# Kernel optimization log

Measured on AMD Instinct MI355X. Metric: run time of the kernel, lower is better.

The kernel has to match this reference:

```python
import jax, jax.numpy as jnp
import numpy as np

DIM = 64
K = 8
B_TAIL = 3.0
HIDDEN = 64
BATCH = 16384
MIN_BIN_WIDTH = 1e-3
MIN_BIN_HEIGHT = 1e-3
MIN_DERIVATIVE = 1e-3


def setup_inputs() -> dict:
    key = jax.random.key(0)
    ks = jax.random.split(key, 8)
    L = DIM - 1
    out_dim = 3 * K - 1
    def u(k, shape, fan_in):
        b = 1.0 / np.sqrt(fan_in)
        return jax.random.uniform(k, shape, minval=-b, maxval=b, dtype=jnp.float32)
    return {
        "x": jax.random.normal(ks[0], (BATCH, DIM), jnp.float32),
        "init_param": jax.random.uniform(ks[1], (out_dim,), minval=-0.5, maxval=0.5, dtype=jnp.float32),
        # conditioner MLP i (i=1..dim-1) maps x[:, :i] -> 3K-1; stacked with zero-masked inputs
        "W1": u(ks[2], (L, HIDDEN, DIM), DIM),
        "b1": u(ks[3], (L, HIDDEN), DIM),
        "W2": u(ks[4], (L, HIDDEN, HIDDEN), HIDDEN),
        "b2": u(ks[5], (L, HIDDEN), HIDDEN),
        "W3": u(ks[6], (L, out_dim, HIDDEN), HIDDEN),
        "b3": u(ks[7], (L, out_dim), HIDDEN),
    }


def _rqs(inputs, uW, uH, uD, left, right):
    # inputs: [D, B]; uW/uH: [D, B, K]; uD: [D, B, K+1] (already edge-padded)
    num_bins = uW.shape[-1]
    widths = jax.nn.softmax(uW, axis=-1)
    widths = MIN_BIN_WIDTH + (1 - MIN_BIN_WIDTH * num_bins) * widths
    cw = jnp.pad(jnp.cumsum(widths, axis=-1), ((0, 0), (0, 0), (1, 0)))
    cw = (right - left) * cw + left
    cw = cw.at[..., 0].set(left).at[..., -1].set(right)
    widths = cw[..., 1:] - cw[..., :-1]

    derivs = MIN_DERIVATIVE + jax.nn.softplus(uD)

    heights = jax.nn.softmax(uH, axis=-1)
    heights = MIN_BIN_HEIGHT + (1 - MIN_BIN_HEIGHT * num_bins) * heights
    ch = jnp.pad(jnp.cumsum(heights, axis=-1), ((0, 0), (0, 0), (1, 0)))
    ch = (right - left) * ch + left  # bottom=left, top=right (symmetric box)
    ch = ch.at[..., 0].set(left).at[..., -1].set(right)
    heights = ch[..., 1:] - ch[..., :-1]

    # searchsorted: sum(inputs >= bin_edges) - 1, with eps on last edge
    cw_s = cw.at[..., -1].add(1e-6)
    bin_idx = jnp.sum(inputs[..., None] >= cw_s, axis=-1) - 1
    bin_idx = jnp.clip(bin_idx, 0, num_bins - 1)[..., None]
    take = lambda a: jnp.take_along_axis(a, bin_idx, axis=-1)[..., 0]

    in_cw = take(cw)
    in_w = take(widths)
    in_ch = take(ch)
    in_h = take(heights)
    in_delta = take(heights / widths)
    d_k = take(derivs)
    d_k1 = take(derivs[..., 1:])

    theta = (inputs - in_cw) / in_w
    t1mt = theta * (1 - theta)
    numer = in_h * (in_delta * theta**2 + d_k * t1mt)
    denom = in_delta + (d_k + d_k1 - 2 * in_delta) * t1mt
    outputs = in_ch + numer / denom
    dnum = in_delta**2 * (d_k1 * theta**2 + 2 * in_delta * t1mt + d_k * (1 - theta) ** 2)
    logabsdet = jnp.log(dnum) - 2 * jnp.log(denom)
    return outputs, logabsdet


def _unconstrained_rqs(inputs, uW, uH, uD, tail_bound):
    inside = (inputs >= -tail_bound) & (inputs <= tail_bound)
    const = float(np.log(np.exp(1 - MIN_DERIVATIVE) - 1))
    uD = jnp.pad(uD, ((0, 0), (0, 0), (1, 1)), constant_values=const)
    x_in = jnp.clip(inputs, -tail_bound, tail_bound)
    out, ld = _rqs(x_in, uW, uH, uD, -tail_bound, tail_bound)
    return jnp.where(inside, out, inputs), jnp.where(inside, ld, 0.0)


def reference(x, init_param, W1, b1, W2, b2, W3, b3):
    Bsz = x.shape[0]
    L = DIM - 1
    # row l of mask keeps x[:, :l+1], zeroes the rest -> identical to per-layer x[:, :i]
    mask = jnp.tril(jnp.ones((L, DIM), x.dtype))
    xm = x[None, :, :] * mask[:, None, :]                         # [L, B, D]
    h = jnp.tanh(jnp.einsum('lbd,lhd->lbh', xm, W1) + b1[:, None, :])
    h = jnp.tanh(jnp.einsum('lbh,lgh->lbg', h, W2) + b2[:, None, :])
    out = jnp.einsum('lbh,loh->lbo', h, W3) + b3[:, None, :]      # [L, B, 3K-1]
    params = jnp.concatenate(
        [jnp.broadcast_to(init_param, (1, Bsz, 3 * K - 1)), out], axis=0)  # [D, B, 3K-1]
    W = 2 * B_TAIL * jax.nn.softmax(params[..., :K], axis=-1)
    H = 2 * B_TAIL * jax.nn.softmax(params[..., K:2 * K], axis=-1)
    Dp = jax.nn.softplus(params[..., 2 * K:])
    z_t, ld = _unconstrained_rqs(x.T, W, H, Dp, B_TAIL)           # [D, B]
    return z_t.T, ld.sum(axis=0)
```

## Files before the change

kernel.cpp:

```cpp
#include <hip/hip_runtime.h>

#define BATCH 16384
#define LAYERS 63
#define BM 128
#define XS 72
#define BLOB_BYTES 21504
#define LDS_OFF 8192
#define LDS_BYTES 13312

typedef float f4 __attribute__((ext_vector_type(4)));
typedef short s8 __attribute__((ext_vector_type(8)));
typedef unsigned int u4 __attribute__((ext_vector_type(4)));

#define LOG2E  1.442695041f
#define LN2    0.6931471806f

__device__ __forceinline__ float rcpf(float v) { return __builtin_amdgcn_rcpf(v); }

__device__ __forceinline__ float exp2_hw(float x) {
#if __has_builtin(__builtin_amdgcn_exp2f)
    return __builtin_amdgcn_exp2f(x);
#else
    return exp2f(x);
#endif
}

__device__ __forceinline__ float fast_tanh(float v) {
    float e = exp2_hw(v * (2.f * LOG2E));
    return 1.f - 2.f * rcpf(e + 1.f);
}
__device__ __forceinline__ float softplus_f(float v) {
    float e = exp2_hw(-fabsf(v) * LOG2E);
    return fmaxf(v, 0.f) + LN2 * __log2f(1.f + e);
}
__device__ __forceinline__ unsigned short f2bf(float f) {
    unsigned int u = __float_as_uint(f);
    u += 0x7fffu + ((u >> 16) & 1u);
    return (unsigned short)(u >> 16);
}
#if __has_builtin(__builtin_amdgcn_cvt_pk_bf16_f32)
__device__ __forceinline__ unsigned pk2(float a, float b) {
    auto r = __builtin_amdgcn_cvt_pk_bf16_f32(a, b);
    return __builtin_bit_cast(unsigned, r);
}
#else
__device__ __forceinline__ unsigned pk2(float a, float b) {
    return (unsigned)f2bf(a) | ((unsigned)f2bf(b) << 16);
}
#endif
__device__ __forceinline__ unsigned long long pack4(float a, float b, float c, float d) {
    return (unsigned long long)pk2(a, b) | ((unsigned long long)pk2(c, d) << 32);
}

__device__ __forceinline__ void rqs_eval(const float* p, float xv, float& zout, float& ldout) {
    const bool inside = (xv >= -3.f) && (xv <= 3.f);
    const float xi = fminf(fmaxf(xv, -3.f), 3.f);

    float wa[8], ha[8];
    {
        float s = 0.f;
        #pragma unroll
        for (int i = 0; i < 8; i++) { wa[i] = exp2_hw(p[i] * LOG2E); s += wa[i]; }
        float inv = 6.f * rcpf(s);
        #pragma unroll
        for (int i = 0; i < 8; i++) wa[i] *= inv;
        s = 0.f;
        #pragma unroll
        for (int i = 0; i < 8; i++) { wa[i] = exp2_hw(wa[i] * LOG2E); s += wa[i]; }
        inv = 0.992f * rcpf(s);
        #pragma unroll
        for (int i = 0; i < 8; i++) wa[i] = 1e-3f + wa[i] * inv;
    }
    {
        float s = 0.f;
        #pragma unroll
        for (int i = 0; i < 8; i++) { ha[i] = exp2_hw(p[8 + i] * LOG2E); s += ha[i]; }
        float inv = 6.f * rcpf(s);
        #pragma unroll
        for (int i = 0; i < 8; i++) ha[i] *= inv;
        s = 0.f;
        #pragma unroll
        for (int i = 0; i < 8; i++) { ha[i] = exp2_hw(ha[i] * LOG2E); s += ha[i]; }
        inv = 0.992f * rcpf(s);
        #pragma unroll
        for (int i = 0; i < 8; i++) ha[i] = 1e-3f + ha[i] * inv;
    }

    float cw[9], ch[9];
    cw[0] = -3.f; ch[0] = -3.f;
    {
        float cs = 0.f, hs = 0.f;
        #pragma unroll
        for (int k = 1; k < 8; k++) {
            cs += wa[k - 1]; cw[k] = 6.f * cs - 3.f;
            hs += ha[k - 1]; ch[k] = 6.f * hs - 3.f;
        }
    }
    cw[8] = 3.f; ch[8] = 3.f;

    int cnt = 0;
    #pragma unroll
    for (int k = 0; k < 8; k++) cnt += (xi >= cw[k]) ? 1 : 0;
    cnt += (xi >= 3.000001f) ? 1 : 0;
    const int bin = min(max(cnt - 1, 0), 7);

    float in_cw = 0.f, in_w = 1.f, in_ch = 0.f, in_h = 1.f;
    float pd0 = 0.f, pd1 = 0.f;
    #pragma unroll
    for (int k = 0; k < 8; k++)
        if (k == bin) {
            in_cw = cw[k]; in_w = cw[k + 1] - cw[k];
            in_ch = ch[k]; in_h = ch[k + 1] - ch[k];
            if (k >= 1) pd0 = p[15 + k];
            if (k <= 6) pd1 = p[16 + k];
        }
    const float dk  = (bin == 0) ? 1.f : 1e-3f + softplus_f(softplus_f(pd0));
    const float dk1 = (bin == 7) ? 1.f : 1e-3f + softplus_f(softplus_f(pd1));

    const float rw    = rcpf(in_w);
    const float delta = in_h * rw;
    const float th    = (xi - in_cw) * rw;
    const float omt = 1.f - th;
    const float t1  = th * omt;
    const float th2 = th * th;
    const float numer = in_h * (delta * th2 + dk * t1);
    const float denom = delta + (dk + dk1 - 2.f * delta) * t1;
    const float rd    = rcpf(denom);
    const float outv  = in_ch + numer * rd;
    const float dnum  = delta * delta * (dk1 * th2 + 2.f * delta * t1 + dk * omt * omt);
    const float ldv = LN2 * __log2f(dnum * rd * rd);

    zout  = inside ? outv : xv;
    ldout = inside ? ldv : 0.f;
}

__global__ __launch_bounds__(256) void prep_kernel(
    const float* __restrict__ x, const float* __restrict__ init_param,
    const float* __restrict__ W1, const float* __restrict__ W2, const float* __restrict__ W3,
    const float* __restrict__ b1, const float* __restrict__ b2, const float* __restrict__ b3,
    unsigned short* __restrict__ x_bf, unsigned char* __restrict__ blobG,
    float* __restrict__ z, float* __restrict__ ld)
{
    const int tid = threadIdx.x;
    if (blockIdx.x < 1024) {
        size_t idx = (size_t)blockIdx.x * 256 + tid;
        f4 v = *(const f4*)&x[idx * 4];
        *(unsigned long long*)&x_bf[idx * 4] = pack4(v[0], v[1], v[2], v[3]);
        return;
    }
    if (blockIdx.x >= 1024 + LAYERS) {
        const int row = (blockIdx.x - 1024 - LAYERS) * 256 + tid;
        float p[23];
        #pragma unroll
        for (int j = 0; j < 23; j++) p[j] = init_param[j];
        float zv, lv;
        rqs_eval(p, x[(size_t)row * 64], zv, lv);
        z[(size_t)row * 64] = zv;
        ld[row] = lv;
        return;
    }
    const int l = blockIdx.x - 1024;
    unsigned char* gb = blobG + (size_t)l * BLOB_BYTES;
    for (int e = tid; e < 1024; e += 256) {
        int m = e >> 9, r = (e >> 3) & 63, j = e & 7;
        const float* src = (m ? W2 : W1) + (size_t)l * 4096 + r * 64 + j * 8;
        unsigned long long lo = pack4(src[0], src[1], src[2], src[3]);
        unsigned long long hi = pack4(src[4], src[5], src[6], src[7]);
        unsigned long long* dst = (unsigned long long*)(gb + m * 8192 + r * 128 + ((j ^ (r & 7)) << 4));
        dst[0] = lo; dst[1] = hi;
    }
    if (tid < 256) {
        int r = tid >> 3, j = tid & 7;
        unsigned long long lo = 0ull, hi = 0ull;
        if (r < 23) {
            const float* src = W3 + (size_t)l * 1472 + r * 64 + j * 8;
            lo = pack4(src[0], src[1], src[2], src[3]);
            hi = pack4(src[4], src[5], src[6], src[7]);
        }
        unsigned long long* dst = (unsigned long long*)(gb + 16384 + r * 128 + ((j ^ (r & 7)) << 4));
        dst[0] = lo; dst[1] = hi;
    }
    if (tid < 64)        *(float*)(gb + 20480 + tid * 4)         = b1[l * 64 + tid];
    else if (tid < 128)  *(float*)(gb + 20736 + (tid - 64) * 4)  = b2[l * 64 + tid - 64];
    else if (tid < 160)  *(float*)(gb + 20992 + (tid - 128) * 4) = (tid - 128 < 23) ? b3[l * 23 + tid - 128] : 0.f;
    else                 { int e = tid - 160; if (e < 96) *(float*)(gb + 21120 + e * 4) = 0.f; }
}

__global__ __launch_bounds__(256, 5) void mlp_rqs_kernel(
    const float* __restrict__ x, const unsigned short* __restrict__ x_bf,
    const unsigned char* __restrict__ blobG,
    float* __restrict__ z, float* __restrict__ ld)
{
    const int l = blockIdx.y, keff = l + 1;
    const int b0 = blockIdx.x * BM;
    const int tid = threadIdx.x;
    const int ln = tid & 63, wv = tid >> 6;
    const int c = ln & 15, q = ln >> 4;
    const int mbase = wv * 32;
    const int c7 = c & 7;

    __shared__ __align__(16) unsigned char blob[LDS_BYTES];
    __shared__ __align__(16) unsigned short Hs[BM * XS];

    unsigned short* W2s = (unsigned short*)blob;
    unsigned short* W3s = (unsigned short*)(blob + 8192);
    const float* b1s = (const float*)(blob + 12288);
    const float* b2s = (const float*)(blob + 12544);
    const float* b3s = (const float*)(blob + 12800);
    float* PsF = (float*)Hs;

    const unsigned char* gblob = blobG + (size_t)l * BLOB_BYTES;

    for (int t = wv; t < 13; t += 4)
        __builtin_amdgcn_global_load_lds(
            (const __attribute__((address_space(1))) void*)(gblob + LDS_OFF + t * 1024 + ln * 16),
            (__attribute__((address_space(3))) void*)(blob + t * 1024 + ln * 16), 16, 0, 0);

    const int ks1 = (keff + 31) >> 5;

    s8 aw1[2][4];
    #pragma unroll
    for (int mt = 0; mt < 4; mt++)
        aw1[0][mt] = *(const s8*)(gblob + (mt * 16 + c) * 128 + ((q ^ c7) << 4));
    if (ks1 == 2) {
        #pragma unroll
        for (int mt = 0; mt < 4; mt++)
            aw1[1][mt] = *(const s8*)(gblob + (mt * 16 + c) * 128 + (((4 + q) ^ c7) << 4));
    }

    u4 B0u, B1u, B2u{}, B3u{};
    {
        const unsigned short* xr = x_bf + (size_t)(b0 + mbase + c) * 64 + q * 8;
        B0u = *(const u4*)xr;  B1u = *(const u4*)(xr + 1024);
        if (ks1 == 2) { B2u = *(const u4*)(xr + 32); B3u = *(const u4*)(xr + 1024 + 32); }
        const int n = keff - ((ks1 - 1) * 32 + q * 8);
        unsigned mk[4];
        #pragma unroll
        for (int i = 0; i < 4; i++) {
            int m = n - 2 * i;
            mk[i] = (m >= 2) ? 0xFFFFFFFFu : ((m == 1) ? 0xFFFFu : 0u);
        }
        if (ks1 == 2) {
            #pragma unroll
            for (int i = 0; i < 4; i++) { B2u[i] &= mk[i]; B3u[i] &= mk[i]; }
        } else {
            #pragma unroll
            for (int i = 0; i < 4; i++) { B0u[i] &= mk[i]; B1u[i] &= mk[i]; }
        }
    }
    const float xv = x[(size_t)(b0 + (tid & 127)) * 64 + keff];

    __syncthreads();

    {
        f4 acc[4][2];
        #pragma unroll
        for (int mt = 0; mt < 4; mt++) {
            f4 bv = *(const f4*)&b1s[mt * 16 + q * 4];
            acc[mt][0] = bv; acc[mt][1] = bv;
        }
        {
            s8 bx0 = __builtin_bit_cast(s8, B0u), bx1 = __builtin_bit_cast(s8, B1u);
            #pragma unroll
            for (int mt = 0; mt < 4; mt++) {
                acc[mt][0] = __builtin_amdgcn_mfma_f32_16x16x32_bf16(aw1[0][mt], bx0, acc[mt][0], 0, 0, 0);
                acc[mt][1] = __builtin_amdgcn_mfma_f32_16x16x32_bf16(aw1[0][mt], bx1, acc[mt][1], 0, 0, 0);
            }
        }
        if (ks1 == 2) {
            s8 bx0 = __builtin_bit_cast(s8, B2u), bx1 = __builtin_bit_cast(s8, B3u);
            #pragma unroll
            for (int mt = 0; mt < 4; mt++) {
                acc[mt][0] = __builtin_amdgcn_mfma_f32_16x16x32_bf16(aw1[1][mt], bx0, acc[mt][0], 0, 0, 0);
                acc[mt][1] = __builtin_amdgcn_mfma_f32_16x16x32_bf16(aw1[1][mt], bx1, acc[mt][1], 0, 0, 0);
            }
        }
        #pragma unroll
        for (int mt = 0; mt < 4; mt++)
            #pragma unroll
            for (int nt = 0; nt < 2; nt++) {
                f4 a = acc[mt][nt];
                unsigned long long w = (unsigned long long)pk2(fast_tanh(a[0]), fast_tanh(a[1]))
                    | ((unsigned long long)pk2(fast_tanh(a[2]), fast_tanh(a[3])) << 32);
                *(unsigned long long*)&Hs[(mbase + nt * 16 + c) * XS + mt * 16 + q * 4] = w;
            }
    }

    {
        f4 acc[4][2];
        #pragma unroll
        for (int mt = 0; mt < 4; mt++) {
            f4 bv = *(const f4*)&b2s[mt * 16 + q * 4];
            acc[mt][0] = bv; acc[mt][1] = bv;
        }
        #pragma unroll
        for (int ks = 0; ks < 2; ks++) {
            s8 bh0 = *(const s8*)&Hs[(mbase + c) * XS + ks * 32 + q * 8];
            s8 bh1 = *(const s8*)&Hs[(mbase + 16 + c) * XS + ks * 32 + q * 8];
            const int sb = ((ks * 4 + q) ^ c7) * 8;
            #pragma unroll
            for (int mt = 0; mt < 4; mt++) {
                s8 aw = *(const s8*)&W2s[(mt * 16 + c) * 64 + sb];
                acc[mt][0] = __builtin_amdgcn_mfma_f32_16x16x32_bf16(aw, bh0, acc[mt][0], 0, 0, 0);
                acc[mt][1] = __builtin_amdgcn_mfma_f32_16x16x32_bf16(aw, bh1, acc[mt][1], 0, 0, 0);
            }
        }
        #pragma unroll
        for (int mt = 0; mt < 4; mt++)
            #pragma unroll
            for (int nt = 0; nt < 2; nt++) {
                f4 a = acc[mt][nt];
                unsigned long long w = (unsigned long long)pk2(fast_tanh(a[0]), fast_tanh(a[1]))
                    | ((unsigned long long)pk2(fast_tanh(a[2]), fast_tanh(a[3])) << 32);
                *(unsigned long long*)&Hs[(mbase + nt * 16 + c) * XS + mt * 16 + q * 4] = w;
            }
    }

    {
        f4 acc3[2][2];
        #pragma unroll
        for (int mt = 0; mt < 2; mt++) {
            f4 bv = *(const f4*)&b3s[mt * 16 + q * 4];
            acc3[mt][0] = bv; acc3[mt][1] = bv;
        }
        #pragma unroll
        for (int ks = 0; ks < 2; ks++) {
            s8 bh0 = *(const s8*)&Hs[(mbase + c) * XS + ks * 32 + q * 8];
            s8 bh1 = *(const s8*)&Hs[(mbase + 16 + c) * XS + ks * 32 + q * 8];
            const int sb = ((ks * 4 + q) ^ c7) * 8;
            #pragma unroll
            for (int mt = 0; mt < 2; mt++) {
                s8 aw = *(const s8*)&W3s[(mt * 16 + c) * 64 + sb];
                acc3[mt][0] = __builtin_amdgcn_mfma_f32_16x16x32_bf16(aw, bh0, acc3[mt][0], 0, 0, 0);
                acc3[mt][1] = __builtin_amdgcn_mfma_f32_16x16x32_bf16(aw, bh1, acc3[mt][1], 0, 0, 0);
            }
        }
        #pragma unroll
        for (int mt = 0; mt < 2; mt++)
            #pragma unroll
            for (int nt = 0; nt < 2; nt++)
                *(f4*)&PsF[(mbase + nt * 16 + c) * 36 + mt * 16 + q * 4] = acc3[mt][nt];
    }
    __syncthreads();

    if (tid < BM) {
        const float* prow = &PsF[tid * 36];
        f4 pv0 = *(const f4*)(prow + 0);
        f4 pv1 = *(const f4*)(prow + 4);
        f4 pv2 = *(const f4*)(prow + 8);
        f4 pv3 = *(const f4*)(prow + 12);

        const bool inside = (xv >= -3.f) && (xv <= 3.f);
        const float xi = fminf(fmaxf(xv, -3.f), 3.f);

        float e[8];
        float s = 0.f;
        #pragma unroll
        for (int i = 0; i < 4; i++) { e[i]     = exp2_hw(pv0[i] * LOG2E); s += e[i]; }
        #pragma unroll
        for (int i = 0; i < 4; i++) { e[4 + i] = exp2_hw(pv1[i] * LOG2E); s += e[4 + i]; }
        float inv2 = (6.f * LOG2E) * rcpf(s);
        float s2 = 0.f;
        #pragma unroll
        for (int i = 0; i < 8; i++) { e[i] = exp2_hw(e[i] * inv2); s2 += e[i]; }
        float inv3 = (6.f * 0.992f) * rcpf(s2);

        float w6k  = 6e-3f + e[0] * inv3;
        float cs   = -3.f + w6k;
        float in_cw = -3.f, in_w = w6k;
        int bin = 0;
        #pragma unroll
        for (int k = 1; k < 8; k++) {
            w6k = 6e-3f + e[k] * inv3;
            const bool ge = (xi >= cs);
            in_cw = ge ? cs  : in_cw;
            in_w  = ge ? w6k : in_w;
            bin   = ge ? k   : bin;
            cs += w6k;
        }

        s = 0.f;
        #pragma unroll
        for (int i = 0; i < 4; i++) { e[i]     = exp2_hw(pv2[i] * LOG2E); s += e[i]; }
        #pragma unroll
        for (int i = 0; i < 4; i++) { e[4 + i] = exp2_hw(pv3[i] * LOG2E); s += e[4 + i]; }
        inv2 = (6.f * LOG2E) * rcpf(s);
        s2 = 0.f;
        #pragma unroll
        for (int i = 0; i < 8; i++) { e[i] = exp2_hw(e[i] * inv2); s2 += e[i]; }
        inv3 = (6.f * 0.992f) * rcpf(s2);

        float h6p = 6e-3f + e[0] * inv3;
        float csh = -3.f, in_ch = -3.f, in_h = h6p;
        #pragma unroll
        for (int k = 1; k < 8; k++) {
            csh += h6p;
            h6p = 6e-3f + e[k] * inv3;
            const bool sel = (bin >= k);
            in_ch = sel ? csh : in_ch;
            in_h  = sel ? h6p : in_h;
        }

        const float pd0 = prow[15 + bin];
        const float pd1 = prow[16 + bin];
        const float dk  = (bin == 0) ? 1.f : 1e-3f + softplus_f(softplus_f(pd0));
        const float dk1 = (bin == 7) ? 1.f : 1e-3f + softplus_f(softplus_f(pd1));

        const float rw    = rcpf(in_w);
        const float delta = in_h * rw;
        const float th    = (xi - in_cw) * rw;
        const float omt = 1.f - th;
        const float t1  = th * omt;
        const float th2 = th * th;
        const float numer = in_h * (delta * th2 + dk * t1);
        const float denom = delta + (dk + dk1 - 2.f * delta) * t1;
        const float rd    = rcpf(denom);
        const float outv  = in_ch + numer * rd;
        const float dnum  = delta * delta * (dk1 * th2 + 2.f * delta * t1 + dk * omt * omt);
        const float ldv = LN2 * __log2f(dnum * rd * rd);

        z[(size_t)(b0 + tid) * 64 + keff] = inside ? outv : xv;
        unsafeAtomicAdd(ld + b0 + tid, inside ? ldv : 0.f);
    }
}

extern "C" void kernel_launch(void* const* d_in, const int* in_sizes, int n_in,
                              void* d_out, int out_size, void* d_ws, size_t ws_size,
                              hipStream_t stream)
{
    const float* x  = (const float*)d_in[0];
    const float* ip = (const float*)d_in[1];
    const float* W1 = (const float*)d_in[2];
    const float* b1 = (const float*)d_in[3];
    const float* W2 = (const float*)d_in[4];
    const float* b2 = (const float*)d_in[5];
    const float* W3 = (const float*)d_in[6];
    const float* b3 = (const float*)d_in[7];

    float* z  = (float*)d_out;
    float* ld = z + (size_t)BATCH * 64;

    unsigned short* x_bf = (unsigned short*)d_ws;
    unsigned char*  blobG = (unsigned char*)(x_bf + (size_t)BATCH * 64);

    prep_kernel<<<1024 + LAYERS + 64, 256, 0, stream>>>(
        x, ip, W1, W2, W3, b1, b2, b3, x_bf, blobG, z, ld);
    mlp_rqs_kernel<<<dim3(BATCH / BM, LAYERS), 256, 0, stream>>>(
        x, x_bf, blobG, z, ld);
}
```

Baseline: 128.2 us.

## Load W2 fragments into registers, shrink LDS blob, simplify softplus chain and tanh

W2 weight fragments are now loaded directly from global memory into registers during layer 1, so they no longer go through LDS. This cuts the staged LDS blob from 13 KB to 5 KB and raises the occupancy hint from 5 to 6 blocks. The double softplus is rewritten algebraically as log(2+e^p), and tanh now uses an exp plus a polynomial instead of a reciprocal. The risks are more register pressure, which could block the higher occupancy, and small accuracy changes from the polynomial tanh.

```diff
diff --git a/kernel.cpp b/kernel.cpp
--- a/kernel.cpp
+++ b/kernel.cpp
@@ -5,8 +5,8 @@
 #define BM 128
 #define XS 72
 #define BLOB_BYTES 21504
-#define LDS_OFF 8192
-#define LDS_BYTES 13312
+#define LDS_OFF 16384
+#define LDS_BYTES 5120
 
 typedef float f4 __attribute__((ext_vector_type(4)));
 typedef short s8 __attribute__((ext_vector_type(8)));
@@ -26,12 +26,18 @@
 }
 
 __device__ __forceinline__ float fast_tanh(float v) {
-    float e = exp2_hw(v * (2.f * LOG2E));
-    return 1.f - 2.f * rcpf(e + 1.f);
-}
-__device__ __forceinline__ float softplus_f(float v) {
-    float e = exp2_hw(-fabsf(v) * LOG2E);
-    return fmaxf(v, 0.f) + LN2 * __log2f(1.f + e);
+    const float u = exp2_hw(fabsf(v) * -2.885390082f);
+    float q = __builtin_fmaf(-0.21528896f, u, 0.85191968f);
+    q = __builtin_fmaf(q, u, -1.55543360f);
+    q = __builtin_fmaf(q, u,  1.91204672f);
+    q = __builtin_fmaf(q, u, -1.99321600f);
+    q = __builtin_fmaf(q, u,  1.99991152f);
+    const float r = __builtin_fmaf(-q, u, 1.f);
+    return __uint_as_float((__float_as_uint(r) & 0x7fffffffu) |
+                           (__float_as_uint(v) & 0x80000000u));
+}
+__device__ __forceinline__ float deriv_chain(float p) {
+    return 1e-3f + LN2 * __log2f(2.f + exp2_hw(p * LOG2E));
 }
 __device__ __forceinline__ unsigned short f2bf(float f) {
     unsigned int u = __float_as_uint(f);
@@ -114,8 +120,8 @@
             if (k >= 1) pd0 = p[15 + k];
             if (k <= 6) pd1 = p[16 + k];
         }
-    const float dk  = (bin == 0) ? 1.f : 1e-3f + softplus_f(softplus_f(pd0));
-    const float dk1 = (bin == 7) ? 1.f : 1e-3f + softplus_f(softplus_f(pd1));
+    const float dk  = (bin == 0) ? 1.f : deriv_chain(pd0);
+    const float dk1 = (bin == 7) ? 1.f : deriv_chain(pd1);
 
     const float rw    = rcpf(in_w);
     const float delta = in_h * rw;
@@ -186,7 +192,7 @@
     else                 { int e = tid - 160; if (e < 96) *(float*)(gb + 21120 + e * 4) = 0.f; }
 }
 
-__global__ __launch_bounds__(256, 5) void mlp_rqs_kernel(
+__global__ __launch_bounds__(256, 6) void mlp_rqs_kernel(
     const float* __restrict__ x, const unsigned short* __restrict__ x_bf,
     const unsigned char* __restrict__ blobG,
     float* __restrict__ z, float* __restrict__ ld)
@@ -202,16 +208,15 @@
     __shared__ __align__(16) unsigned char blob[LDS_BYTES];
     __shared__ __align__(16) unsigned short Hs[BM * XS];
 
-    unsigned short* W2s = (unsigned short*)blob;
-    unsigned short* W3s = (unsigned short*)(blob + 8192);
-    const float* b1s = (const float*)(blob + 12288);
-    const float* b2s = (const float*)(blob + 12544);
-    const float* b3s = (const float*)(blob + 12800);
+    unsigned short* W3s = (unsigned short*)blob;
+    const float* b1s = (const float*)(blob + 4096);
+    const float* b2s = (const float*)(blob + 4352);
+    const float* b3s = (const float*)(blob + 4608);
     float* PsF = (float*)Hs;
 
     const unsigned char* gblob = blobG + (size_t)l * BLOB_BYTES;
 
-    for (int t = wv; t < 13; t += 4)
+    for (int t = wv; t < 5; t += 4)
         __builtin_amdgcn_global_load_lds(
             (const __attribute__((address_space(1))) void*)(gblob + LDS_OFF + t * 1024 + ln * 16),
             (__attribute__((address_space(3))) void*)(blob + t * 1024 + ln * 16), 16, 0, 0);
@@ -252,6 +257,8 @@
 
     __syncthreads();
 
+    s8 aw2[2][4];
+
     {
         f4 acc[4][2];
         #pragma unroll
@@ -275,6 +282,13 @@
                 acc[mt][1] = __builtin_amdgcn_mfma_f32_16x16x32_bf16(aw1[1][mt], bx1, acc[mt][1], 0, 0, 0);
             }
         }
+
+        #pragma unroll
+        for (int ks = 0; ks < 2; ks++)
+            #pragma unroll
+            for (int mt = 0; mt < 4; mt++)
+                aw2[ks][mt] = *(const s8*)(gblob + 8192 + (mt * 16 + c) * 128 + (((ks * 4 + q) ^ c7) << 4));
+
         #pragma unroll
         for (int mt = 0; mt < 4; mt++)
             #pragma unroll
@@ -297,12 +311,10 @@
         for (int ks = 0; ks < 2; ks++) {
             s8 bh0 = *(const s8*)&Hs[(mbase + c) * XS + ks * 32 + q * 8];
             s8 bh1 = *(const s8*)&Hs[(mbase + 16 + c) * XS + ks * 32 + q * 8];
-            const int sb = ((ks * 4 + q) ^ c7) * 8;
             #pragma unroll
             for (int mt = 0; mt < 4; mt++) {
-                s8 aw = *(const s8*)&W2s[(mt * 16 + c) * 64 + sb];
-                acc[mt][0] = __builtin_amdgcn_mfma_f32_16x16x32_bf16(aw, bh0, acc[mt][0], 0, 0, 0);
-                acc[mt][1] = __builtin_amdgcn_mfma_f32_16x16x32_bf16(aw, bh1, acc[mt][1], 0, 0, 0);
+                acc[mt][0] = __builtin_amdgcn_mfma_f32_16x16x32_bf16(aw2[ks][mt], bh0, acc[mt][0], 0, 0, 0);
+                acc[mt][1] = __builtin_amdgcn_mfma_f32_16x16x32_bf16(aw2[ks][mt], bh1, acc[mt][1], 0, 0, 0);
             }
         }
         #pragma unroll
@@ -403,8 +415,8 @@
 
         const float pd0 = prow[15 + bin];
         const float pd1 = prow[16 + bin];
-        const float dk  = (bin == 0) ? 1.f : 1e-3f + softplus_f(softplus_f(pd0));
-        const float dk1 = (bin == 7) ? 1.f : 1e-3f + softplus_f(softplus_f(pd1));
+        const float dk  = (bin == 0) ? 1.f : deriv_chain(pd0);
+        const float dk1 = (bin == 7) ? 1.f : deriv_chain(pd1);
 
         const float rw    = rcpf(in_w);
         const float delta = in_h * rw;
```

Result: slower. 135.9 us (+6.0%).
